# Kernel tuning notes

Measured on AMD Instinct MI355X. Metric: run time of the kernel, lower is better.

The kernel has to match this reference:

```python
import jax, jax.numpy as jnp
import numpy as np

DIM = 2048
N_EXPERTS = 32
TOPK = 4
INTER = 1024
ROUTE_SCALE = 1.0


def setup_inputs() -> dict:
    key = jax.random.key(0)
    ks = jax.random.split(key, 8)
    s = 0.02  # realistic init scale for weights
    return {
        "x": jax.random.normal(ks[0], (2, 2048, DIM), dtype=jnp.float32),
        "gate_w": jax.random.normal(ks[1], (N_EXPERTS, DIM), dtype=jnp.float32) * s,
        "w1": jax.random.normal(ks[2], (N_EXPERTS, INTER, DIM), dtype=jnp.float32) * s,
        "w2": jax.random.normal(ks[3], (N_EXPERTS, DIM, INTER), dtype=jnp.float32) * s,
        "w3": jax.random.normal(ks[4], (N_EXPERTS, INTER, DIM), dtype=jnp.float32) * s,
        "sw1": jax.random.normal(ks[5], (2 * INTER, DIM), dtype=jnp.float32) * s,
        "sw2": jax.random.normal(ks[6], (DIM, 2 * INTER), dtype=jnp.float32) * s,
        "sw3": jax.random.normal(ks[7], (2 * INTER, DIM), dtype=jnp.float32) * s,
    }


def reference(x, gate_w, w1, w2, w3, sw1, sw2, sw3):
    shape = x.shape
    xf = x.reshape(-1, DIM)                       # [T, D]
    T = xf.shape[0]

    # --- Gate: softmax scores, top-k routing (n_groups == 1 path) ---
    scores = jax.nn.softmax(xf @ gate_w.T, axis=-1)          # [T, E]
    weights, indices = jax.lax.top_k(scores, TOPK)           # [T, K]
    weights = weights * ROUTE_SCALE

    # Dense combine weights: w_full[t, e] = routing weight if expert e chosen
    w_full = jnp.zeros((T, N_EXPERTS), dtype=xf.dtype)
    w_full = w_full.at[jnp.arange(T)[:, None], indices].add(weights)  # [T, E]

    # --- Routed experts: SwiGLU FFN per expert, weighted combine ---
    def body(y, inp):
        w1e, w2e, w3e, we = inp                   # [I,D], [D,I], [I,D], [T]
        h = jax.nn.silu(xf @ w1e.T) * (xf @ w3e.T)  # [T, I]
        return y + (h @ w2e.T) * we[:, None], None

    y0 = jnp.zeros_like(xf)
    y, _ = jax.lax.scan(body, y0, (w1, w2, w3, w_full.T))

    # --- Shared experts (dense SwiGLU MLP over all tokens) ---
    z = (jax.nn.silu(xf @ sw1.T) * (xf @ sw3.T)) @ sw2.T

    return (y + z).reshape(shape)
```

## Files before the change

### kernel.cpp

```cpp
#include <hip/hip_runtime.h>
#include <cstdint>
#include <cstddef>

#define DIMD   2048
#define NEXP   32
#define TOPKK  4
#define INTERI 1024
#define TTOK   4096
#define NSLOT  (TTOK*TOPKK)

typedef short bf16x8 __attribute__((ext_vector_type(8)));
typedef float f32x4  __attribute__((ext_vector_type(4)));

__device__ __forceinline__ unsigned short f2bf(float f){
  unsigned int u = __float_as_uint(f);
  u = (u + 0x7FFFu + ((u >> 16) & 1u)) >> 16;
  return (unsigned short)u;
}
__device__ __forceinline__ unsigned int pk2(float a, float b){
  return (unsigned int)f2bf(a) | ((unsigned int)f2bf(b) << 16);
}
__device__ __forceinline__ uint4 pack8(const float4& a, const float4& b){
  return make_uint4(pk2(a.x,a.y), pk2(a.z,a.w), pk2(b.x,b.y), pk2(b.z,b.w));
}

__global__ __launch_bounds__(64) void gate_kernel(
    const float* __restrict__ x, const float* __restrict__ gw,
    int* __restrict__ topk_i, float* __restrict__ topk_w, int* __restrict__ counts)
{
  int t = blockIdx.x;
  int lane = threadIdx.x;
  const float* xr = x + (size_t)t * DIMD;
  float xv[32];
  #pragma unroll
  for (int j = 0; j < 32; j++) xv[j] = xr[lane + 64*j];

  float myscore = -1e30f;
  for (int e = 0; e < NEXP; e++){
    const float* we = gw + (size_t)e * DIMD;
    float p = 0.f;
    #pragma unroll
    for (int j = 0; j < 32; j++) p += xv[j] * we[lane + 64*j];
    #pragma unroll
    for (int s = 32; s > 0; s >>= 1) p += __shfl_xor(p, s, 64);
    if (lane == e) myscore = p;
  }
  float v = (lane < NEXP) ? myscore : -1e30f;
  float m = v;
  #pragma unroll
  for (int s = 32; s > 0; s >>= 1) m = fmaxf(m, __shfl_xor(m, s, 64));
  float ev = (lane < NEXP) ? __expf(v - m) : 0.f;
  float ssum = ev;
  #pragma unroll
  for (int s = 32; s > 0; s >>= 1) ssum += __shfl_xor(ssum, s, 64);
  float prob = (lane < NEXP) ? (ev / ssum) : -1.f;

  float pcur = prob;
  for (int k = 0; k < TOPKK; k++){
    float bv = pcur; int bi = lane;
    #pragma unroll
    for (int s = 32; s > 0; s >>= 1){
      float ov = __shfl_xor(bv, s, 64);
      int   oi = __shfl_xor(bi, s, 64);
      if (ov > bv || (ov == bv && oi < bi)){ bv = ov; bi = oi; }
    }
    if (lane == 0){
      topk_i[t*TOPKK + k] = bi;
      topk_w[t*TOPKK + k] = bv;
      atomicAdd(&counts[bi], 1);
    }
    if (lane == bi) pcur = -1.f;
  }
}

__global__ void scan_kernel(const int* __restrict__ counts, int* __restrict__ offsets,
                            int* __restrict__ cursor)
{
  if (threadIdx.x == 0){
    int acc = 0;
    for (int e = 0; e < NEXP; e++){ offsets[e] = acc; acc += counts[e]; }
    offsets[NEXP] = acc;
  }
  if (threadIdx.x < NEXP) cursor[threadIdx.x] = 0;
}

__global__ __launch_bounds__(256) void build_kernel(
    const int* __restrict__ topk_i, const float* __restrict__ topk_w,
    const int* __restrict__ offsets, int* __restrict__ cursor,
    int* __restrict__ slot_token, float* __restrict__ slot_w)
{
  int t = blockIdx.x * blockDim.x + threadIdx.x;
  if (t >= TTOK) return;
  for (int k = 0; k < TOPKK; k++){
    int e = topk_i[t*TOPKK + k];
    int pos = atomicAdd(&cursor[e], 1);
    int s = offsets[e] + pos;
    slot_token[s] = t;
    slot_w[s] = topk_w[t*TOPKK + k];
  }
}

__global__ __launch_bounds__(256) void cvt_kernel(
    const float* __restrict__ x, unsigned short* __restrict__ xb, int n)
{
  int i = (blockIdx.x * blockDim.x + threadIdx.x) * 8;
  if (i >= n) return;
  const float4* p = (const float4*)(x + i);
  float4 a = p[0], b = p[1];
  *(uint4*)(xb + i) = pack8(a, b);
}

#define BM  128
#define BN  64
#define BKG 64
#define LDA 72

__global__ __launch_bounds__(256) void gemm1_dual(
    const unsigned short* __restrict__ xb,
    const float* __restrict__ W1g, const float* __restrict__ W3g,
    const int* __restrict__ slot_token, const float* __restrict__ slot_w,
    const int* __restrict__ offsets,
    unsigned short* __restrict__ H, int Ncols, int routed)
{
  __shared__ unsigned short As[BM*LDA];
  __shared__ unsigned short Bs1[BN*LDA];
  __shared__ unsigned short Bs3[BN*LDA];
  __shared__ int   rowtok[BM];
  __shared__ float roww[BM];

  int e = blockIdx.z;
  int seg0, segn;
  const float *W1, *W3;
  if (routed){
    seg0 = offsets[e]; segn = offsets[e+1] - seg0;
    W1 = W1g + (size_t)e * INTERI * DIMD;
    W3 = W3g + (size_t)e * INTERI * DIMD;
  } else {
    seg0 = 0; segn = TTOK; W1 = W1g; W3 = W3g;
  }
  int m0 = blockIdx.y * BM;
  if (m0 >= segn) return;
  int rows = min(BM, segn - m0);
  int n0 = blockIdx.x * BN;
  int tid = threadIdx.x;

  if (tid < BM){
    int r = tid;
    if (r < rows){
      int g = seg0 + m0 + r;
      rowtok[r] = routed ? slot_token[g] : g;
      roww[r]   = routed ? slot_w[g] : 1.0f;
    } else { rowtok[r] = -1; roww[r] = 0.f; }
  }
  __syncthreads();

  f32x4 zz = {0.f, 0.f, 0.f, 0.f};
  f32x4 acc1[4][2], acc3[4][2];
  #pragma unroll
  for (int i = 0; i < 4; i++)
    #pragma unroll
    for (int j = 0; j < 2; j++){ acc1[i][j] = zz; acc3[i][j] = zz; }

  int wv = tid >> 6, lane = tid & 63;
  int wm = wv >> 1, wn = wv & 1;
  int l15 = lane & 15, quad = lane >> 4;

  int ar = tid >> 1, ac = (tid & 1) * 32;
  int br = tid >> 2, bc = (tid & 3) * 16;
  int tok = rowtok[ar];

  for (int k0 = 0; k0 < DIMD; k0 += BKG){
    uint4 av[4];
    av[0] = av[1] = av[2] = av[3] = make_uint4(0,0,0,0);
    if (tok >= 0){
      const uint4* p = (const uint4*)(xb + (size_t)tok * DIMD + k0 + ac);
      av[0] = p[0]; av[1] = p[1]; av[2] = p[2]; av[3] = p[3];
    }
    const float4* b1p = (const float4*)(W1 + (size_t)(n0 + br) * DIMD + k0 + bc);
    const float4* b3p = (const float4*)(W3 + (size_t)(n0 + br) * DIMD + k0 + bc);
    float4 b1v0 = b1p[0], b1v1 = b1p[1], b1v2 = b1p[2], b1v3 = b1p[3];
    float4 b3v0 = b3p[0], b3v1 = b3p[1], b3v2 = b3p[2], b3v3 = b3p[3];

    __syncthreads();
    {
      uint4* aw = (uint4*)&As[ar*LDA + ac];
      aw[0] = av[0]; aw[1] = av[1]; aw[2] = av[2]; aw[3] = av[3];
      uint4* b1w = (uint4*)&Bs1[br*LDA + bc];
      b1w[0] = pack8(b1v0, b1v1); b1w[1] = pack8(b1v2, b1v3);
      uint4* b3w = (uint4*)&Bs3[br*LDA + bc];
      b3w[0] = pack8(b3v0, b3v1); b3w[1] = pack8(b3v2, b3v3);
    }
    __syncthreads();

    #pragma unroll
    for (int ks = 0; ks < 2; ks++){
      bf16x8 af[4];
      #pragma unroll
      for (int im = 0; im < 4; im++)
        af[im] = *(const bf16x8*)&As[(wm*64 + im*16 + l15)*LDA + ks*32 + quad*8];
      bf16x8 b1f[2], b3f[2];
      #pragma unroll
      for (int in = 0; in < 2; in++){
        b1f[in] = *(const bf16x8*)&Bs1[(wn*32 + in*16 + l15)*LDA + ks*32 + quad*8];
        b3f[in] = *(const bf16x8*)&Bs3[(wn*32 + in*16 + l15)*LDA + ks*32 + quad*8];
      }
      #pragma unroll
      for (int im = 0; im < 4; im++)
        #pragma unroll
        for (int in = 0; in < 2; in++){
          acc1[im][in] = __builtin_amdgcn_mfma_f32_16x16x32_bf16(af[im], b1f[in], acc1[im][in], 0, 0, 0);
          acc3[im][in] = __builtin_amdgcn_mfma_f32_16x16x32_bf16(af[im], b3f[in], acc3[im][in], 0, 0, 0);
        }
    }
  }

  #pragma unroll
  for (int im = 0; im < 4; im++){
    #pragma unroll
    for (int in = 0; in < 2; in++){
      int col = n0 + wn*32 + in*16 + l15;
      #pragma unroll
      for (int reg = 0; reg < 4; reg++){
        int rr = wm*64 + im*16 + quad*4 + reg;
        if (rr < rows){
          float v1 = acc1[im][in][reg];
          float v3 = acc3[im][in][reg];
          float hv = (v1 / (1.f + __expf(-v1))) * v3 * roww[rr];
          H[(size_t)(seg0 + m0 + rr) * Ncols + col] = f2bf(hv);
        }
      }
    }
  }
}

#define BN2 128
__global__ __launch_bounds__(256) void gemm2_kernel(
    const unsigned short* __restrict__ Hsrc, const float* __restrict__ W2g,
    const int* __restrict__ slot_token, const int* __restrict__ offsets,
    float* __restrict__ out, int Kd, int routed)
{
  __shared__ unsigned short As[BM*LDA];
  __shared__ unsigned short Bs[BN2*LDA];
  __shared__ int rowtok[BM];

  int e = blockIdx.z;
  int seg0, segn;
  const float* W2;
  if (routed){
    seg0 = offsets[e]; segn = offsets[e+1] - seg0;
    W2 = W2g + (size_t)e * DIMD * INTERI;
  } else {
    seg0 = 0; segn = TTOK; W2 = W2g;
  }
  int m0 = blockIdx.y * BM;
  if (m0 >= segn) return;
  int rows = min(BM, segn - m0);
  int n0 = blockIdx.x * BN2;
  int tid = threadIdx.x;

  if (tid < BM){
    int r = tid;
    rowtok[r] = (r < rows) ? (routed ? slot_token[seg0 + m0 + r] : (m0 + r)) : -1;
  }
  __syncthreads();

  f32x4 zz = {0.f,0.f,0.f,0.f};
  f32x4 acc[4][4];
  #pragma unroll
  for (int i = 0; i < 4; i++)
    #pragma unroll
    for (int j = 0; j < 4; j++) acc[i][j] = zz;

  int wv = tid >> 6, lane = tid & 63;
  int wm = wv >> 1, wn = wv & 1;
  int l15 = lane & 15, quad = lane >> 4;

  int ar = tid >> 1, ac = (tid & 1) * 32;
  int brr = tid >> 1, bc = (tid & 1) * 32;
  bool aok = (ar < rows);

  for (int k0 = 0; k0 < Kd; k0 += BKG){
    uint4 av[4];
    av[0] = av[1] = av[2] = av[3] = make_uint4(0,0,0,0);
    if (aok){
      const uint4* p = (const uint4*)(Hsrc + (size_t)(seg0 + m0 + ar) * Kd + k0 + ac);
      av[0] = p[0]; av[1] = p[1]; av[2] = p[2]; av[3] = p[3];
    }
    const float4* bp = (const float4*)(W2 + (size_t)(n0 + brr) * Kd + k0 + bc);
    float4 bv0 = bp[0], bv1 = bp[1], bv2 = bp[2], bv3 = bp[3];
    float4 bv4 = bp[4], bv5 = bp[5], bv6 = bp[6], bv7 = bp[7];

    __syncthreads();
    {
      uint4* aw = (uint4*)&As[ar*LDA + ac];
      aw[0] = av[0]; aw[1] = av[1]; aw[2] = av[2]; aw[3] = av[3];
      uint4* bw = (uint4*)&Bs[brr*LDA + bc];
      bw[0] = pack8(bv0, bv1); bw[1] = pack8(bv2, bv3);
      bw[2] = pack8(bv4, bv5); bw[3] = pack8(bv6, bv7);
    }
    __syncthreads();

    #pragma unroll
    for (int ks = 0; ks < 2; ks++){
      bf16x8 af[4], bfr[4];
      #pragma unroll
      for (int im = 0; im < 4; im++)
        af[im] = *(const bf16x8*)&As[(wm*64 + im*16 + l15)*LDA + ks*32 + quad*8];
      #pragma unroll
      for (int in = 0; in < 4; in++)
        bfr[in] = *(const bf16x8*)&Bs[(wn*64 + in*16 + l15)*LDA + ks*32 + quad*8];
      #pragma unroll
      for (int im = 0; im < 4; im++)
        #pragma unroll
        for (int in = 0; in < 4; in++)
          acc[im][in] = __builtin_amdgcn_mfma_f32_16x16x32_bf16(af[im], bfr[in], acc[im][in], 0, 0, 0);
    }
  }

  #pragma unroll
  for (int im = 0; im < 4; im++){
    #pragma unroll
    for (int in = 0; in < 4; in++){
      int col = n0 + wn*64 + in*16 + l15;
      #pragma unroll
      for (int reg = 0; reg < 4; reg++){
        int rr = wm*64 + im*16 + quad*4 + reg;
        if (rr < rows){
          int orow = rowtok[rr];
          float v = acc[im][in][reg];
          if (routed) atomicAdd(&out[(size_t)orow * DIMD + col], v);
          else        out[(size_t)orow * DIMD + col] += v;
        }
      }
    }
  }
}

extern "C" void kernel_launch(void* const* d_in, const int* in_sizes, int n_in,
                              void* d_out, int out_size, void* d_ws, size_t ws_size,
                              hipStream_t stream)
{
  const float* x      = (const float*)d_in[0];
  const float* gate_w = (const float*)d_in[1];
  const float* w1     = (const float*)d_in[2];
  const float* w2     = (const float*)d_in[3];
  const float* w3     = (const float*)d_in[4];
  const float* sw1    = (const float*)d_in[5];
  const float* sw2    = (const float*)d_in[6];
  const float* sw3    = (const float*)d_in[7];
  float* out = (float*)d_out;

  char* w = (char*)d_ws;
  unsigned short* xb = (unsigned short*)(w);
  unsigned short* h  = (unsigned short*)(w + 16777216);
  unsigned short* h2 = (unsigned short*)(w + 50331648);
  int*   slot_token  = (int*)  (w + 67108864);
  float* slot_w      = (float*)(w + 67174400);
  int*   topk_i      = (int*)  (w + 67239936);
  float* topk_w      = (float*)(w + 67305472);
  int*   counts      = (int*)  (w + 67371008);
  int*   cursor      = (int*)  (w + 67371136);
  int*   offsets     = (int*)  (w + 67371264);

  hipMemsetAsync(out, 0, (size_t)TTOK * DIMD * sizeof(float), stream);
  hipMemsetAsync(counts, 0, NEXP * sizeof(int), stream);

  gate_kernel<<<TTOK, 64, 0, stream>>>(x, gate_w, topk_i, topk_w, counts);
  scan_kernel<<<1, 64, 0, stream>>>(counts, offsets, cursor);
  build_kernel<<<TTOK/256, 256, 0, stream>>>(topk_i, topk_w, offsets, cursor, slot_token, slot_w);
  cvt_kernel<<<(TTOK*DIMD)/(256*8), 256, 0, stream>>>(x, xb, TTOK*DIMD);

  gemm1_dual<<<dim3(INTERI/BN, 32, NEXP), 256, 0, stream>>>(
      xb, w1, w3, slot_token, slot_w, offsets, h, INTERI, 1);
  gemm2_kernel<<<dim3(DIMD/BN2, 32, NEXP), 256, 0, stream>>>(
      h, w2, slot_token, offsets, out, INTERI, 1);

  gemm1_dual<<<dim3(2*INTERI/BN, TTOK/BM, 1), 256, 0, stream>>>(
      xb, sw1, sw3, nullptr, nullptr, offsets, h2, 2*INTERI, 0);
  gemm2_kernel<<<dim3(DIMD/BN2, TTOK/BM, 1), 256, 0, stream>>>(
      h2, sw2, nullptr, offsets, out, 2*INTERI, 0);
}
```

Before: 1.525 ms.

## Pre-convert weights to bf16 and stage tiles via global_load_lds with XOR swizzle

When the workspace is large enough, all expert and shared weights are converted to bf16 in separate passes so the GEMMs can stream bf16 tiles directly into LDS with global_load_lds. Padded LDS rows are replaced by an XOR-swizzled layout to avoid bank conflicts. The shared-expert path now runs first and writes out directly, which removes the output memset, and the two H buffers are merged into one. The extra conversion passes read about 800MB of fp32 weights on every call, which may cost more than the fp32 loads and in-kernel packing they replace.

```diff
diff --git a/kernel.cpp b/kernel.cpp
--- a/kernel.cpp
+++ b/kernel.cpp
@@ -7,10 +7,10 @@
 #define TOPKK  4
 #define INTERI 1024
 #define TTOK   4096
-#define NSLOT  (TTOK*TOPKK)
 
 typedef short bf16x8 __attribute__((ext_vector_type(8)));
 typedef float f32x4  __attribute__((ext_vector_type(4)));
+typedef unsigned int u32;
 
 __device__ __forceinline__ unsigned short f2bf(float f){
   unsigned int u = __float_as_uint(f);
@@ -22,6 +22,12 @@
 }
 __device__ __forceinline__ uint4 pack8(const float4& a, const float4& b){
   return make_uint4(pk2(a.x,a.y), pk2(a.z,a.w), pk2(b.x,b.y), pk2(b.z,b.w));
+}
+
+__device__ __forceinline__ void gl_lds16(const void* g, void* l){
+  __builtin_amdgcn_global_load_lds(
+      (const __attribute__((address_space(1))) u32*)g,
+      (__attribute__((address_space(3))) u32*)l, 16, 0, 0);
 }
 
 __global__ __launch_bounds__(64) void gate_kernel(
@@ -101,94 +107,115 @@
 }
 
 __global__ __launch_bounds__(256) void cvt_kernel(
-    const float* __restrict__ x, unsigned short* __restrict__ xb, int n)
+    const float* __restrict__ src, unsigned short* __restrict__ dst, int n)
 {
   int i = (blockIdx.x * blockDim.x + threadIdx.x) * 8;
   if (i >= n) return;
-  const float4* p = (const float4*)(x + i);
+  const float4* p = (const float4*)(src + i);
   float4 a = p[0], b = p[1];
-  *(uint4*)(xb + i) = pack8(a, b);
-}
-
-#define BM  128
-#define BN  64
-#define BKG 64
-#define LDA 72
-
-__global__ __launch_bounds__(256) void gemm1_dual(
+  *(uint4*)(dst + i) = pack8(a, b);
+}
+
+template<bool WB16>
+__global__ __launch_bounds__(256) void gemm1_v2(
     const unsigned short* __restrict__ xb,
-    const float* __restrict__ W1g, const float* __restrict__ W3g,
+    const void* __restrict__ W1g, const void* __restrict__ W3g,
     const int* __restrict__ slot_token, const float* __restrict__ slot_w,
     const int* __restrict__ offsets,
     unsigned short* __restrict__ H, int Ncols, int routed)
 {
-  __shared__ unsigned short As[BM*LDA];
-  __shared__ unsigned short Bs1[BN*LDA];
-  __shared__ unsigned short Bs3[BN*LDA];
-  __shared__ int   rowtok[BM];
-  __shared__ float roww[BM];
+  __shared__ unsigned short As[128*64];
+  __shared__ unsigned short Bs1[64*64];
+  __shared__ unsigned short Bs3[64*64];
+  __shared__ float roww[128];
 
   int e = blockIdx.z;
   int seg0, segn;
-  const float *W1, *W3;
-  if (routed){
-    seg0 = offsets[e]; segn = offsets[e+1] - seg0;
-    W1 = W1g + (size_t)e * INTERI * DIMD;
-    W3 = W3g + (size_t)e * INTERI * DIMD;
+  if (routed){ seg0 = offsets[e]; segn = offsets[e+1] - seg0; }
+  else       { seg0 = 0; segn = TTOK; }
+  int m0 = blockIdx.y * 128;
+  if (m0 >= segn) return;
+  int rows = min(128, segn - m0);
+  int n0 = blockIdx.x * 64;
+  int tid = threadIdx.x, wv = tid >> 6, lane = tid & 63;
+
+  size_t woff = routed ? (size_t)e * INTERI * DIMD : 0;
+  const unsigned short* W1h = nullptr; const unsigned short* W3h = nullptr;
+  const float* W1f = nullptr; const float* W3f = nullptr;
+  if constexpr (WB16){
+    W1h = (const unsigned short*)W1g + woff;
+    W3h = (const unsigned short*)W3g + woff;
   } else {
-    seg0 = 0; segn = TTOK; W1 = W1g; W3 = W3g;
-  }
-  int m0 = blockIdx.y * BM;
-  if (m0 >= segn) return;
-  int rows = min(BM, segn - m0);
-  int n0 = blockIdx.x * BN;
-  int tid = threadIdx.x;
-
-  if (tid < BM){
-    int r = tid;
-    if (r < rows){
-      int g = seg0 + m0 + r;
-      rowtok[r] = routed ? slot_token[g] : g;
-      roww[r]   = routed ? slot_w[g] : 1.0f;
-    } else { rowtok[r] = -1; roww[r] = 0.f; }
-  }
-  __syncthreads();
-
-  f32x4 zz = {0.f, 0.f, 0.f, 0.f};
+    W1f = (const float*)W1g + woff;
+    W3f = (const float*)W3g + woff;
+  }
+
+  if (tid < 128)
+    roww[tid] = (tid < rows) ? (routed ? slot_w[seg0 + m0 + tid] : 1.0f) : 0.f;
+
+  int sub = lane >> 3, cst = lane & 7;
+  int swz = cst ^ sub;
+
+  const unsigned short* agp[4];
+  #pragma unroll
+  for (int t = 0; t < 4; t++){
+    int r = wv*32 + t*8 + sub;
+    int rc = (r < rows) ? r : 0;
+    int tok = routed ? slot_token[seg0 + m0 + rc] : (m0 + rc);
+    agp[t] = xb + (size_t)tok * DIMD + swz*8;
+  }
+  const unsigned short* bg1[2]; const unsigned short* bg3[2];
+  if constexpr (WB16){
+    #pragma unroll
+    for (int t = 0; t < 2; t++){
+      int r = wv*16 + t*8 + sub;
+      bg1[t] = W1h + (size_t)(n0 + r) * DIMD + swz*8;
+      bg3[t] = W3h + (size_t)(n0 + r) * DIMD + swz*8;
+    }
+  }
+
+  f32x4 zz = {0.f,0.f,0.f,0.f};
   f32x4 acc1[4][2], acc3[4][2];
   #pragma unroll
   for (int i = 0; i < 4; i++)
     #pragma unroll
     for (int j = 0; j < 2; j++){ acc1[i][j] = zz; acc3[i][j] = zz; }
 
-  int wv = tid >> 6, lane = tid & 63;
   int wm = wv >> 1, wn = wv & 1;
   int l15 = lane & 15, quad = lane >> 4;
 
-  int ar = tid >> 1, ac = (tid & 1) * 32;
-  int br = tid >> 2, bc = (tid & 3) * 16;
-  int tok = rowtok[ar];
-
-  for (int k0 = 0; k0 < DIMD; k0 += BKG){
-    uint4 av[4];
-    av[0] = av[1] = av[2] = av[3] = make_uint4(0,0,0,0);
-    if (tok >= 0){
-      const uint4* p = (const uint4*)(xb + (size_t)tok * DIMD + k0 + ac);
-      av[0] = p[0]; av[1] = p[1]; av[2] = p[2]; av[3] = p[3];
-    }
-    const float4* b1p = (const float4*)(W1 + (size_t)(n0 + br) * DIMD + k0 + bc);
-    const float4* b3p = (const float4*)(W3 + (size_t)(n0 + br) * DIMD + k0 + bc);
-    float4 b1v0 = b1p[0], b1v1 = b1p[1], b1v2 = b1p[2], b1v3 = b1p[3];
-    float4 b3v0 = b3p[0], b3v1 = b3p[1], b3v2 = b3p[2], b3v3 = b3p[3];
-
+  for (int k0 = 0; k0 < DIMD; k0 += 64){
+    float4 v1a[2], v1b[2], v3a[2], v3b[2];
+    if constexpr (!WB16){
+      #pragma unroll
+      for (int s = 0; s < 2; s++){
+        int m = tid + s*256;
+        int r = m >> 3, c = m & 7;
+        int clog = c ^ (r & 7);
+        const float4* p1 = (const float4*)(W1f + (size_t)(n0 + r)*DIMD + k0 + clog*8);
+        const float4* p3 = (const float4*)(W3f + (size_t)(n0 + r)*DIMD + k0 + clog*8);
+        v1a[s] = p1[0]; v1b[s] = p1[1];
+        v3a[s] = p3[0]; v3b[s] = p3[1];
+      }
+    }
     __syncthreads();
-    {
-      uint4* aw = (uint4*)&As[ar*LDA + ac];
-      aw[0] = av[0]; aw[1] = av[1]; aw[2] = av[2]; aw[3] = av[3];
-      uint4* b1w = (uint4*)&Bs1[br*LDA + bc];
-      b1w[0] = pack8(b1v0, b1v1); b1w[1] = pack8(b1v2, b1v3);
-      uint4* b3w = (uint4*)&Bs3[br*LDA + bc];
-      b3w[0] = pack8(b3v0, b3v1); b3w[1] = pack8(b3v2, b3v3);
+    #pragma unroll
+    for (int t = 0; t < 4; t++)
+      gl_lds16(agp[t] + k0, &As[(wv*32 + t*8) * 64]);
+    if constexpr (WB16){
+      #pragma unroll
+      for (int t = 0; t < 2; t++){
+        gl_lds16(bg1[t] + k0, &Bs1[(wv*16 + t*8) * 64]);
+        gl_lds16(bg3[t] + k0, &Bs3[(wv*16 + t*8) * 64]);
+      }
+    } else {
+      #pragma unroll
+      for (int s = 0; s < 2; s++){
+        int m = tid + s*256;
+        int r = m >> 3, c = m & 7;
+        *(uint4*)&Bs1[r*64 + c*8] = pack8(v1a[s], v1b[s]);
+        *(uint4*)&Bs3[r*64 + c*8] = pack8(v3a[s], v3b[s]);
+      }
     }
     __syncthreads();
 
@@ -196,13 +223,18 @@
     for (int ks = 0; ks < 2; ks++){
       bf16x8 af[4];
       #pragma unroll
-      for (int im = 0; im < 4; im++)
-        af[im] = *(const bf16x8*)&As[(wm*64 + im*16 + l15)*LDA + ks*32 + quad*8];
+      for (int im = 0; im < 4; im++){
+        int row = wm*64 + im*16 + l15;
+        int pc = (ks*4 + quad) ^ (l15 & 7);
+        af[im] = *(const bf16x8*)&As[row*64 + pc*8];
+      }
       bf16x8 b1f[2], b3f[2];
       #pragma unroll
       for (int in = 0; in < 2; in++){
-        b1f[in] = *(const bf16x8*)&Bs1[(wn*32 + in*16 + l15)*LDA + ks*32 + quad*8];
-        b3f[in] = *(const bf16x8*)&Bs3[(wn*32 + in*16 + l15)*LDA + ks*32 + quad*8];
+        int row = wn*32 + in*16 + l15;
+        int pc = (ks*4 + quad) ^ (l15 & 7);
+        b1f[in] = *(const bf16x8*)&Bs1[row*64 + pc*8];
+        b3f[in] = *(const bf16x8*)&Bs3[row*64 + pc*8];
       }
       #pragma unroll
       for (int im = 0; im < 4; im++)
@@ -233,36 +265,52 @@
   }
 }
 
-#define BN2 128
-__global__ __launch_bounds__(256) void gemm2_kernel(
-    const unsigned short* __restrict__ Hsrc, const float* __restrict__ W2g,
+template<bool WB16>
+__global__ __launch_bounds__(256) void gemm2_v2(
+    const unsigned short* __restrict__ Hsrc, const void* __restrict__ W2g,
     const int* __restrict__ slot_token, const int* __restrict__ offsets,
     float* __restrict__ out, int Kd, int routed)
 {
-  __shared__ unsigned short As[BM*LDA];
-  __shared__ unsigned short Bs[BN2*LDA];
-  __shared__ int rowtok[BM];
+  __shared__ unsigned short As[128*64];
+  __shared__ unsigned short Bs[128*64];
+  __shared__ int rowtok[128];
 
   int e = blockIdx.z;
   int seg0, segn;
-  const float* W2;
-  if (routed){
-    seg0 = offsets[e]; segn = offsets[e+1] - seg0;
-    W2 = W2g + (size_t)e * DIMD * INTERI;
-  } else {
-    seg0 = 0; segn = TTOK; W2 = W2g;
-  }
-  int m0 = blockIdx.y * BM;
+  if (routed){ seg0 = offsets[e]; segn = offsets[e+1] - seg0; }
+  else       { seg0 = 0; segn = TTOK; }
+  int m0 = blockIdx.y * 128;
   if (m0 >= segn) return;
-  int rows = min(BM, segn - m0);
-  int n0 = blockIdx.x * BN2;
-  int tid = threadIdx.x;
-
-  if (tid < BM){
-    int r = tid;
-    rowtok[r] = (r < rows) ? (routed ? slot_token[seg0 + m0 + r] : (m0 + r)) : -1;
-  }
-  __syncthreads();
+  int rows = min(128, segn - m0);
+  int n0 = blockIdx.x * 128;
+  int tid = threadIdx.x, wv = tid >> 6, lane = tid & 63;
+
+  size_t woff = routed ? (size_t)e * DIMD * INTERI : 0;
+  const unsigned short* W2h = nullptr; const float* W2f = nullptr;
+  if constexpr (WB16) W2h = (const unsigned short*)W2g + woff;
+  else                W2f = (const float*)W2g + woff;
+
+  if (tid < 128)
+    rowtok[tid] = (tid < rows) ? (routed ? slot_token[seg0 + m0 + tid] : (m0 + tid)) : -1;
+
+  int sub = lane >> 3, cst = lane & 7;
+  int swz = cst ^ sub;
+
+  const unsigned short* agp[4];
+  #pragma unroll
+  for (int t = 0; t < 4; t++){
+    int r = wv*32 + t*8 + sub;
+    int rc = (r < rows) ? r : 0;
+    agp[t] = Hsrc + (size_t)(seg0 + m0 + rc) * Kd + swz*8;
+  }
+  const unsigned short* bgp[4];
+  if constexpr (WB16){
+    #pragma unroll
+    for (int t = 0; t < 4; t++){
+      int r = wv*32 + t*8 + sub;
+      bgp[t] = W2h + (size_t)(n0 + r) * Kd + swz*8;
+    }
+  }
 
   f32x4 zz = {0.f,0.f,0.f,0.f};
   f32x4 acc[4][4];
@@ -271,32 +319,36 @@
     #pragma unroll
     for (int j = 0; j < 4; j++) acc[i][j] = zz;
 
-  int wv = tid >> 6, lane = tid & 63;
   int wm = wv >> 1, wn = wv & 1;
   int l15 = lane & 15, quad = lane >> 4;
 
-  int ar = tid >> 1, ac = (tid & 1) * 32;
-  int brr = tid >> 1, bc = (tid & 1) * 32;
-  bool aok = (ar < rows);
-
-  for (int k0 = 0; k0 < Kd; k0 += BKG){
-    uint4 av[4];
-    av[0] = av[1] = av[2] = av[3] = make_uint4(0,0,0,0);
-    if (aok){
-      const uint4* p = (const uint4*)(Hsrc + (size_t)(seg0 + m0 + ar) * Kd + k0 + ac);
-      av[0] = p[0]; av[1] = p[1]; av[2] = p[2]; av[3] = p[3];
-    }
-    const float4* bp = (const float4*)(W2 + (size_t)(n0 + brr) * Kd + k0 + bc);
-    float4 bv0 = bp[0], bv1 = bp[1], bv2 = bp[2], bv3 = bp[3];
-    float4 bv4 = bp[4], bv5 = bp[5], bv6 = bp[6], bv7 = bp[7];
-
+  for (int k0 = 0; k0 < Kd; k0 += 64){
+    float4 bva[4], bvb[4];
+    if constexpr (!WB16){
+      #pragma unroll
+      for (int s = 0; s < 4; s++){
+        int m = tid + s*256;
+        int r = m >> 3, c = m & 7;
+        int clog = c ^ (r & 7);
+        const float4* p = (const float4*)(W2f + (size_t)(n0 + r)*Kd + k0 + clog*8);
+        bva[s] = p[0]; bvb[s] = p[1];
+      }
+    }
     __syncthreads();
-    {
-      uint4* aw = (uint4*)&As[ar*LDA + ac];
-      aw[0] = av[0]; aw[1] = av[1]; aw[2] = av[2]; aw[3] = av[3];
-      uint4* bw = (uint4*)&Bs[brr*LDA + bc];
-      bw[0] = pack8(bv0, bv1); bw[1] = pack8(bv2, bv3);
-      bw[2] = pack8(bv4, bv5); bw[3] = pack8(bv6, bv7);
+    #pragma unroll
+    for (int t = 0; t < 4; t++)
+      gl_lds16(agp[t] + k0, &As[(wv*32 + t*8) * 64]);
+    if constexpr (WB16){
+      #pragma unroll
+      for (int t = 0; t < 4; t++)
+        gl_lds16(bgp[t] + k0, &Bs[(wv*32 + t*8) * 64]);
+    } else {
+      #pragma unroll
+      for (int s = 0; s < 4; s++){
+        int m = tid + s*256;
+        int r = m >> 3, c = m & 7;
+        *(uint4*)&Bs[r*64 + c*8] = pack8(bva[s], bvb[s]);
+      }
     }
     __syncthreads();
 
@@ -304,11 +356,17 @@
     for (int ks = 0; ks < 2; ks++){
       bf16x8 af[4], bfr[4];
       #pragma unroll
-      for (int im = 0; im < 4; im++)
-        af[im] = *(const bf16x8*)&As[(wm*64 + im*16 + l15)*LDA + ks*32 + quad*8];
-      #pragma unroll
-      for (int in = 0; in < 4; in++)
-        bfr[in] = *(const bf16x8*)&Bs[(wn*64 + in*16 + l15)*LDA + ks*32 + quad*8];
+      for (int im = 0; im < 4; im++){
+        int row = wm*64 + im*16 + l15;
+        int pc = (ks*4 + quad) ^ (l15 & 7);
+        af[im] = *(const bf16x8*)&As[row*64 + pc*8];
+      }
+      #pragma unroll
+      for (int in = 0; in < 4; in++){
+        int row = wn*64 + in*16 + l15;
+        int pc = (ks*4 + quad) ^ (l15 & 7);
+        bfr[in] = *(const bf16x8*)&Bs[row*64 + pc*8];
+      }
       #pragma unroll
       for (int im = 0; im < 4; im++)
         #pragma unroll
@@ -329,7 +387,7 @@
           int orow = rowtok[rr];
           float v = acc[im][in][reg];
           if (routed) atomicAdd(&out[(size_t)orow * DIMD + col], v);
-          else        out[(size_t)orow * DIMD + col] += v;
+          else        out[(size_t)orow * DIMD + col] = v;
         }
       }
     }
@@ -350,19 +408,42 @@
   const float* sw3    = (const float*)d_in[7];
   float* out = (float*)d_out;
 
+  const size_t SZ_WE = (size_t)NEXP * INTERI * DIMD * 2;
+  const size_t SZ_SW = (size_t)2*INTERI * DIMD * 2;
+  const size_t SZ_XB = (size_t)TTOK * DIMD * 2;
+  const size_t SZ_H  = (size_t)TTOK * TOPKK * INTERI * 2;
+  const size_t META  = 1u << 20;
+  const size_t NEED  = 3*SZ_WE + 3*SZ_SW + SZ_XB + SZ_H + META;
+
   char* w = (char*)d_ws;
-  unsigned short* xb = (unsigned short*)(w);
-  unsigned short* h  = (unsigned short*)(w + 16777216);
-  unsigned short* h2 = (unsigned short*)(w + 50331648);
-  int*   slot_token  = (int*)  (w + 67108864);
-  float* slot_w      = (float*)(w + 67174400);
-  int*   topk_i      = (int*)  (w + 67239936);
-  float* topk_w      = (float*)(w + 67305472);
-  int*   counts      = (int*)  (w + 67371008);
-  int*   cursor      = (int*)  (w + 67371136);
-  int*   offsets     = (int*)  (w + 67371264);
-
-  hipMemsetAsync(out, 0, (size_t)TTOK * DIMD * sizeof(float), stream);
+  bool big = (ws_size >= NEED);
+
+  unsigned short *w1b=0, *w3b=0, *w2b=0, *sw1b=0, *sw3b=0, *sw2b=0, *xb, *h;
+  char* meta;
+  if (big){
+    size_t o = 0;
+    w1b  = (unsigned short*)(w + o); o += SZ_WE;
+    w3b  = (unsigned short*)(w + o); o += SZ_WE;
+    w2b  = (unsigned short*)(w + o); o += SZ_WE;
+    sw1b = (unsigned short*)(w + o); o += SZ_SW;
+    sw3b = (unsigned short*)(w + o); o += SZ_SW;
+    sw2b = (unsigned short*)(w + o); o += SZ_SW;
+    xb   = (unsigned short*)(w + o); o += SZ_XB;
+    h    = (unsigned short*)(w + o); o += SZ_H;
+    meta = w + o;
+  } else {
+    xb   = (unsigned short*)(w);
+    h    = (unsigned short*)(w + SZ_XB);
+    meta = w + SZ_XB + SZ_H;
+  }
+  int*   slot_token = (int*)  (meta);
+  float* slot_w     = (float*)(meta + 65536);
+  int*   topk_i     = (int*)  (meta + 131072);
+  float* topk_w     = (float*)(meta + 196608);
+  int*   counts     = (int*)  (meta + 262144);
+  int*   cursor     = (int*)  (meta + 262272);
+  int*   offsets    = (int*)  (meta + 262400);
+
   hipMemsetAsync(counts, 0, NEXP * sizeof(int), stream);
 
   gate_kernel<<<TTOK, 64, 0, stream>>>(x, gate_w, topk_i, topk_w, counts);
@@ -370,13 +451,32 @@
   build_kernel<<<TTOK/256, 256, 0, stream>>>(topk_i, topk_w, offsets, cursor, slot_token, slot_w);
   cvt_kernel<<<(TTOK*DIMD)/(256*8), 256, 0, stream>>>(x, xb, TTOK*DIMD);
 
-  gemm1_dual<<<dim3(INTERI/BN, 32, NEXP), 256, 0, stream>>>(
-      xb, w1, w3, slot_token, slot_w, offsets, h, INTERI, 1);
-  gemm2_kernel<<<dim3(DIMD/BN2, 32, NEXP), 256, 0, stream>>>(
-      h, w2, slot_token, offsets, out, INTERI, 1);
-
-  gemm1_dual<<<dim3(2*INTERI/BN, TTOK/BM, 1), 256, 0, stream>>>(
-      xb, sw1, sw3, nullptr, nullptr, offsets, h2, 2*INTERI, 0);
-  gemm2_kernel<<<dim3(DIMD/BN2, TTOK/BM, 1), 256, 0, stream>>>(
-      h2, sw2, nullptr, offsets, out, 2*INTERI, 0);
-}
+  if (big){
+    const int NWE = NEXP * INTERI * DIMD;
+    const int NSW = 2*INTERI * DIMD;
+    cvt_kernel<<<NWE/(256*8), 256, 0, stream>>>(w1,  w1b,  NWE);
+    cvt_kernel<<<NWE/(256*8), 256, 0, stream>>>(w3,  w3b,  NWE);
+    cvt_kernel<<<NWE/(256*8), 256, 0, stream>>>(w2,  w2b,  NWE);
+    cvt_kernel<<<NSW/(256*8), 256, 0, stream>>>(sw1, sw1b, NSW);
+    cvt_kernel<<<NSW/(256*8), 256, 0, stream>>>(sw3, sw3b, NSW);
+    cvt_kernel<<<NSW/(256*8), 256, 0, stream>>>(sw2, sw2b, NSW);
+
+    gemm1_v2<true><<<dim3(2*INTERI/64, TTOK/128, 1), 256, 0, stream>>>(
+        xb, sw1b, sw3b, nullptr, nullptr, offsets, h, 2*INTERI, 0);
+    gemm2_v2<true><<<dim3(DIMD/128, TTOK/128, 1), 256, 0, stream>>>(
+        h, sw2b, nullptr, offsets, out, 2*INTERI, 0);
+    gemm1_v2<true><<<dim3(INTERI/64, 32, NEXP), 256, 0, stream>>>(
+        xb, w1b, w3b, slot_token, slot_w, offsets, h, INTERI, 1);
+    gemm2_v2<true><<<dim3(DIMD/128, 32, NEXP), 256, 0, stream>>>(
+        h, w2b, slot_token, offsets, out, INTERI, 1);
+  } else {
+    gemm1_v2<false><<<dim3(2*INTERI/64, TTOK/128, 1), 256, 0, stream>>>(
+        xb, sw1, sw3, nullptr, nullptr, offsets, h, 2*INTERI, 0);
+    gemm2_v2<false><<<dim3(DIMD/128, TTOK/128, 1), 256, 0, stream>>>(
+        h, sw2, nullptr, offsets, out, 2*INTERI, 0);
+    gemm1_v2<false><<<dim3(INTERI/64, 32, NEXP), 256, 0, stream>>>(
+        xb, w1, w3, slot_token, slot_w, offsets, h, INTERI, 1);
+    gemm2_v2<false><<<dim3(DIMD/128, 32, NEXP), 256, 0, stream>>>(
+        h, w2, slot_token, offsets, out, INTERI, 1);
+  }
+}
```

New measurement: 1.505 ms. About the same (-1.3%).
